# Optimization experiments

Hardware: AMD Instinct MI355X
Metric: run time of the kernel (lower is better)

## Reference

```python
import jax, jax.numpy as jnp
import numpy as np

B, S, E, H = 2, 2048, 512, 8
D = E // H  # head size = 64
LN_EPS = 1e-5


def setup_inputs() -> dict:
    key = jax.random.key(0)
    ks = jax.random.split(key, 8)
    s_in = 1.0 / np.sqrt(E)
    return {
        "x": jax.random.normal(ks[0], (B, S, E), jnp.float32),
        # per-head projection weights, stored [H, E, D] so q = x @ Wq[h]
        "Wq": jax.random.normal(ks[1], (H, E, D), jnp.float32) * s_in,
        "Wk": jax.random.normal(ks[2], (H, E, D), jnp.float32) * s_in,
        "Wv": jax.random.normal(ks[3], (H, E, D), jnp.float32) * s_in,
        "Wp": jax.random.normal(ks[4], (E, E), jnp.float32) * s_in,
        "bp": jnp.zeros((E,), jnp.float32),
        "gamma": jnp.ones((E,), jnp.float32),
        "beta": jnp.zeros((E,), jnp.float32),
        # causal mask buffer: masked_fill where mask == 0
        "mask": jnp.tril(jnp.ones((S, S), jnp.int32)),
    }


def reference(x, Wq, Wk, Wv, Wp, bp, gamma, beta, mask):
    # batched per-head projections (equivalent to the H small Linears)
    q = jnp.einsum("bse,hed->bhsd", x, Wq)
    k = jnp.einsum("bse,hed->bhsd", x, Wk)
    v = jnp.einsum("bse,hed->bhsd", x, Wv)
    # NOTE: original has NO 1/sqrt(d) scaling
    att_log = jnp.einsum("bhsd,bhtd->bhst", q, k)
    att_log = jnp.where(mask == 0, -jnp.inf, att_log)
    att = jax.nn.softmax(att_log, axis=-1)
    o = jnp.einsum("bhst,bhtd->bhsd", att, v)  # [B,H,S,D]
    # torch.cat((val, values)) prepends each head -> final order head H-1 .. 0
    o = o[:, ::-1]
    vals = o.transpose(0, 2, 1, 3).reshape(B, S, E)
    out = vals @ Wp.T + bp + x
    mu = jnp.mean(out, axis=-1, keepdims=True)
    var = jnp.var(out, axis=-1, keepdims=True)
    return (out - mu) * jax.lax.rsqrt(var + LN_EPS) * gamma + beta
```

## Files before the change

### kernel.cpp

```cpp
#include <hip/hip_runtime.h>

constexpr int Bn = 2;
constexpr int Sn = 2048;
constexpr int En = 512;
constexpr int Hn = 8;
constexpr int Dn = 64;
constexpr int Mn = Bn * Sn;

typedef short bf8 __attribute__((ext_vector_type(8)));
typedef float f32x4 __attribute__((ext_vector_type(4)));

constexpr size_t XY = (size_t)Mn * En;
constexpr size_t WT = (size_t)3 * En * En;
constexpr size_t WP = (size_t)En * En;
constexpr size_t PL = (size_t)Bn * Hn * Sn * Dn;

__device__ __forceinline__ unsigned short f2bf(float f) {
    unsigned int u = __float_as_uint(f);
    unsigned int r = 0x7FFFu + ((u >> 16) & 1u);
    return (unsigned short)((u + r) >> 16);
}
__device__ __forceinline__ float bf2f(unsigned short u) {
    return __uint_as_float(((unsigned int)u) << 16);
}
__device__ __forceinline__ void split2(float f, unsigned short& hi, unsigned short& lo) {
    hi = f2bf(f);
    lo = f2bf(f - bf2f(hi));
}

__global__ __launch_bounds__(256)
void prep(const float* __restrict__ x, const float* __restrict__ Wp,
          const float* __restrict__ Wq, const float* __restrict__ Wk,
          const float* __restrict__ Wv,
          unsigned short* __restrict__ xh, unsigned short* __restrict__ xl,
          unsigned short* __restrict__ Wph, unsigned short* __restrict__ Wpl,
          unsigned short* __restrict__ Wth, unsigned short* __restrict__ Wtl)
{
    __shared__ float t[64][65];
    const int bid = blockIdx.x;
    const int tid = threadIdx.x;

    if (bid < 1152) {
        const float* src = (bid < 1024) ? x : Wp;
        unsigned short* hp = (bid < 1024) ? xh : Wph;
        unsigned short* lp = (bid < 1024) ? xl : Wpl;
        const int blk = (bid < 1024) ? bid : (bid - 1024);
        const size_t base = ((size_t)blk * 256 + tid) * 8;
        float a[8];
        *(float4*)&a[0] = *(const float4*)(src + base);
        *(float4*)&a[4] = *(const float4*)(src + base + 4);
        unsigned short h[8], l[8];
        #pragma unroll
        for (int j = 0; j < 8; ++j) split2(a[j], h[j], l[j]);
        *(bf8*)(hp + base) = *(bf8*)&h[0];
        *(bf8*)(lp + base) = *(bf8*)&l[0];
        return;
    }

    const int idx = bid - 1152;
    const int ph = idx >> 3;
    const int proj = ph >> 3, h = ph & 7;
    const int e0 = (idx & 7) * 64;
    const float* W = (proj == 0) ? Wq : (proj == 1) ? Wk : Wv;
    const float* src = W + (size_t)h * En * Dn + (size_t)e0 * Dn;

    const int er = tid >> 2, cg = (tid & 3) * 16;
    #pragma unroll
    for (int c = 0; c < 4; ++c) {
        float4 v = *(const float4*)(src + (size_t)er * Dn + cg + 4 * c);
        t[er][cg + 4 * c + 0] = v.x;
        t[er][cg + 4 * c + 1] = v.y;
        t[er][cg + 4 * c + 2] = v.z;
        t[er][cg + 4 * c + 3] = v.w;
    }
    __syncthreads();

    const int d = tid >> 2, jg = (tid & 3) * 16;
    unsigned short h16[16], l16[16];
    #pragma unroll
    for (int j = 0; j < 16; ++j) split2(t[jg + j][d], h16[j], l16[j]);
    const size_t n = (size_t)proj * 512 + h * 64 + d;
    unsigned short* dh = Wth + n * En + e0 + jg;
    unsigned short* dl = Wtl + n * En + e0 + jg;
    *(bf8*)dh       = *(bf8*)&h16[0];
    *(bf8*)(dh + 8) = *(bf8*)&h16[8];
    *(bf8*)dl       = *(bf8*)&l16[0];
    *(bf8*)(dl + 8) = *(bf8*)&l16[8];
}

__global__ __launch_bounds__(256)
void qkv_gemm(const unsigned short* __restrict__ xh,
              const unsigned short* __restrict__ xl,
              const unsigned short* __restrict__ Wth,
              const unsigned short* __restrict__ Wtl,
              unsigned short* __restrict__ qh_g,
              unsigned short* __restrict__ ql_g,
              unsigned short* __restrict__ kh_g,
              unsigned short* __restrict__ kl_g,
              unsigned short* __restrict__ vT_g)
{
    __shared__ __align__(16) unsigned char smraw[40960];
    unsigned short (*Ah)[40] = (unsigned short(*)[40])(smraw);
    unsigned short (*Al)[40] = (unsigned short(*)[40])(smraw + 10240);
    unsigned short (*Bh)[40] = (unsigned short(*)[40])(smraw + 20480);
    unsigned short (*Bl)[40] = (unsigned short(*)[40])(smraw + 30720);
    float (*Cf)[132] = (float(*)[132])(smraw);

    const int tid = threadIdx.x;
    const int m0 = blockIdx.x * 128;
    const int n0 = blockIdx.y * 128;
    const int proj = n0 >> 9;
    const int within = n0 & 511;

    const int wave = tid >> 6, lane = tid & 63;
    const int wm = (wave >> 1) * 64, wn = (wave & 1) * 64;
    const int lm = lane & 15, quad = lane >> 4;

    const int am = tid >> 1;
    const int aks = (tid & 1) * 16;
    const unsigned short* arh = xh + (size_t)(m0 + am) * En + aks;
    const unsigned short* arl = xl + (size_t)(m0 + am) * En + aks;

    const int nn = tid & 127;
    const int bkg = (tid >> 7) * 16;
    const unsigned short* brh = Wth + (size_t)(n0 + nn) * En + bkg;
    const unsigned short* brl = Wtl + (size_t)(n0 + nn) * En + bkg;

    f32x4 acc[4][4];
    #pragma unroll
    for (int i = 0; i < 4; ++i)
        #pragma unroll
        for (int j = 0; j < 4; ++j) acc[i][j] = (f32x4){0.f, 0.f, 0.f, 0.f};

    for (int k0 = 0; k0 < En; k0 += 32) {
        *(bf8*)&Ah[am][aks]     = *(const bf8*)(arh + k0);
        *(bf8*)&Ah[am][aks + 8] = *(const bf8*)(arh + k0 + 8);
        *(bf8*)&Al[am][aks]     = *(const bf8*)(arl + k0);
        *(bf8*)&Al[am][aks + 8] = *(const bf8*)(arl + k0 + 8);
        *(bf8*)&Bh[nn][bkg]     = *(const bf8*)(brh + k0);
        *(bf8*)&Bh[nn][bkg + 8] = *(const bf8*)(brh + k0 + 8);
        *(bf8*)&Bl[nn][bkg]     = *(const bf8*)(brl + k0);
        *(bf8*)&Bl[nn][bkg + 8] = *(const bf8*)(brl + k0 + 8);
        __syncthreads();

        bf8 a_h[4], a_l[4], b_h[4], b_l[4];
        #pragma unroll
        for (int mi = 0; mi < 4; ++mi) {
            a_h[mi] = *(const bf8*)&Ah[wm + mi * 16 + lm][quad * 8];
            a_l[mi] = *(const bf8*)&Al[wm + mi * 16 + lm][quad * 8];
        }
        #pragma unroll
        for (int ni = 0; ni < 4; ++ni) {
            b_h[ni] = *(const bf8*)&Bh[wn + ni * 16 + lm][quad * 8];
            b_l[ni] = *(const bf8*)&Bl[wn + ni * 16 + lm][quad * 8];
        }
        #pragma unroll
        for (int mi = 0; mi < 4; ++mi)
            #pragma unroll
            for (int ni = 0; ni < 4; ++ni) {
                acc[mi][ni] = __builtin_amdgcn_mfma_f32_16x16x32_bf16(a_h[mi], b_h[ni], acc[mi][ni], 0, 0, 0);
                acc[mi][ni] = __builtin_amdgcn_mfma_f32_16x16x32_bf16(a_h[mi], b_l[ni], acc[mi][ni], 0, 0, 0);
                acc[mi][ni] = __builtin_amdgcn_mfma_f32_16x16x32_bf16(a_l[mi], b_h[ni], acc[mi][ni], 0, 0, 0);
            }
        __syncthreads();
    }

    if (proj < 2) {
        unsigned short* hp = (proj == 0) ? qh_g : kh_g;
        unsigned short* lp = (proj == 0) ? ql_g : kl_g;
        #pragma unroll
        for (int p = 0; p < 2; ++p) {
            #pragma unroll
            for (int dmi = 0; dmi < 2; ++dmi) {
                const int mi = 2 * p + dmi;
                #pragma unroll
                for (int ni = 0; ni < 4; ++ni)
                    #pragma unroll
                    for (int r = 0; r < 4; ++r)
                        Cf[(wave >> 1) * 32 + dmi * 16 + quad * 4 + r]
                          [wn + ni * 16 + lm] = acc[mi][ni][r];
            }
            __syncthreads();
            {
                const int lr = tid & 63;
                const int cg = (tid >> 6) * 32;
                const int m = m0 + 64 * (lr >> 5) + 32 * p + 16 * ((lr >> 4) & 1) + (lr & 15);
                const int b = m >> 11, s = m & 2047;
                const int ng = within + cg;
                const int h = ng >> 6, d = ng & 63;
                unsigned short hi[32], lo[32];
                #pragma unroll
                for (int j4 = 0; j4 < 8; ++j4) {
                    float4 v = *(const float4*)&Cf[lr][cg + 4 * j4];
                    split2(v.x, hi[4 * j4 + 0], lo[4 * j4 + 0]);
                    split2(v.y, hi[4 * j4 + 1], lo[4 * j4 + 1]);
                    split2(v.z, hi[4 * j4 + 2], lo[4 * j4 + 2]);
                    split2(v.w, hi[4 * j4 + 3], lo[4 * j4 + 3]);
                }
                const size_t base = (((size_t)(b * Hn + h) * Sn + s) * Dn) + d;
                #pragma unroll
                for (int c = 0; c < 4; ++c) {
                    *(bf8*)(hp + base + 8 * c) = *(bf8*)&hi[8 * c];
                    *(bf8*)(lp + base + 8 * c) = *(bf8*)&lo[8 * c];
                }
            }
            __syncthreads();
        }
    } else {
        #pragma unroll
        for (int mi = 0; mi < 4; ++mi) {
            const int s0 = m0 + wm + mi * 16 + quad * 4;
            const int b = s0 >> 11, s = s0 & 2047;
            #pragma unroll
            for (int ni = 0; ni < 4; ++ni) {
                const int nl = within + wn + ni * 16 + lm;
                const int h = nl >> 6, d = nl & 63;
                ushort4 pk;
                pk.x = f2bf(acc[mi][ni][0]);
                pk.y = f2bf(acc[mi][ni][1]);
                pk.z = f2bf(acc[mi][ni][2]);
                pk.w = f2bf(acc[mi][ni][3]);
                *(ushort4*)(vT_g + ((size_t)(b * Hn + h) * Dn + d) * Sn + s) = pk;
            }
        }
    }
}

__global__ __launch_bounds__(256)
void attn(const unsigned short* __restrict__ qh_g,
          const unsigned short* __restrict__ ql_g,
          const unsigned short* __restrict__ kh_g,
          const unsigned short* __restrict__ kl_g,
          const unsigned short* __restrict__ vT_g,
          unsigned short* __restrict__ Op,
          float* __restrict__ ml)
{
    extern __shared__ unsigned short sm[];
    unsigned short (*khs)[72] = (unsigned short(*)[72])(sm);
    unsigned short (*kls)[72] = (unsigned short(*)[72])(sm + 4608);
    unsigned short (*vTs)[72] = (unsigned short(*)[72])(sm + 9216);
    unsigned short (*pts)[72] = (unsigned short(*)[72])(sm + 13824);
    float* alf = (float*)(sm + 18432);

    const int bidx = blockIdx.x;
    const int r_ = bidx & 255, quarter = bidx >> 8;
    const int a_ = r_ >> 4, bh = r_ & 15;
    const int qt = (quarter & 1) ? (31 - a_) : a_;
    const int hf = quarter >> 1;
    const int n0 = (qt + 2) >> 1;
    const int its = hf ? n0 : 0;
    const int ite = hf ? (qt + 1) : n0;
    const int pslot = hf * 512 + bh * 32 + qt;

    const int tid = threadIdx.x;
    const int wave = tid >> 6, lane = tid & 63;
    const int quad = lane >> 4, lq = lane & 15;

    const unsigned short* khb = kh_g + (size_t)bh * Sn * Dn;
    const unsigned short* klb = kl_g + (size_t)bh * Sn * Dn;
    const unsigned short* vTb = vT_g + (size_t)bh * Dn * Sn;

    bf8 qfh[2], qfl[2];
    {
        const size_t qoff = ((size_t)bh * Sn + (size_t)qt * 64 + wave * 16 + lq) * Dn;
        #pragma unroll
        for (int c = 0; c < 2; ++c) {
            qfh[c] = *(const bf8*)(qh_g + qoff + c * 32 + quad * 8);
            qfl[c] = *(const bf8*)(ql_g + qoff + c * 32 + quad * 8);
        }
    }

    f32x4 accO[4];
    #pragma unroll
    for (int nj = 0; nj < 4; ++nj) accO[nj] = (f32x4){0.f, 0.f, 0.f, 0.f};
    float m = -1e30f, l = 0.f;

    const int srow = tid & 63;
    const int sdg  = tid >> 6;

    bf8 pk0, pk1, pl0, pl1, pv0, pv1;
    if (its < ite) {
        const int t0 = its * 64;
        const unsigned short* kr = khb + (size_t)(t0 + srow) * Dn + sdg * 16;
        const unsigned short* lr = klb + (size_t)(t0 + srow) * Dn + sdg * 16;
        const unsigned short* vr = vTb + (size_t)srow * Sn + t0 + sdg * 16;
        pk0 = *(const bf8*)(kr);  pk1 = *(const bf8*)(kr + 8);
        pl0 = *(const bf8*)(lr);  pl1 = *(const bf8*)(lr + 8);
        pv0 = *(const bf8*)(vr);  pv1 = *(const bf8*)(vr + 8);
    }

    for (int it = its; it < ite; ++it) {
        __syncthreads();
        *(bf8*)&khs[srow][sdg * 16]     = pk0;
        *(bf8*)&khs[srow][sdg * 16 + 8] = pk1;
        *(bf8*)&kls[srow][sdg * 16]     = pl0;
        *(bf8*)&kls[srow][sdg * 16 + 8] = pl1;
        *(bf8*)&vTs[srow][sdg * 16]     = pv0;
        *(bf8*)&vTs[srow][sdg * 16 + 8] = pv1;
        __syncthreads();

        if (it + 1 < ite) {
            const int t1 = (it + 1) * 64;
            const unsigned short* kr = khb + (size_t)(t1 + srow) * Dn + sdg * 16;
            const unsigned short* lr = klb + (size_t)(t1 + srow) * Dn + sdg * 16;
            const unsigned short* vr = vTb + (size_t)srow * Sn + t1 + sdg * 16;
            pk0 = *(const bf8*)(kr);  pk1 = *(const bf8*)(kr + 8);
            pl0 = *(const bf8*)(lr);  pl1 = *(const bf8*)(lr + 8);
            pv0 = *(const bf8*)(vr);  pv1 = *(const bf8*)(vr + 8);
        }

        f32x4 accS[4];
        #pragma unroll
        for (int mi = 0; mi < 4; ++mi) accS[mi] = (f32x4){0.f, 0.f, 0.f, 0.f};
        #pragma unroll
        for (int mi = 0; mi < 4; ++mi) {
            #pragma unroll
            for (int c = 0; c < 2; ++c) {
                bf8 ah = *(const bf8*)&khs[mi * 16 + lq][c * 32 + quad * 8];
                bf8 al = *(const bf8*)&kls[mi * 16 + lq][c * 32 + quad * 8];
                accS[mi] = __builtin_amdgcn_mfma_f32_16x16x32_bf16(ah, qfh[c], accS[mi], 0, 0, 0);
                accS[mi] = __builtin_amdgcn_mfma_f32_16x16x32_bf16(ah, qfl[c], accS[mi], 0, 0, 0);
                accS[mi] = __builtin_amdgcn_mfma_f32_16x16x32_bf16(al, qfh[c], accS[mi], 0, 0, 0);
            }
        }

        if (it == qt) {
            const int qrel = wave * 16 + lq;
            #pragma unroll
            for (int mi = 0; mi < 4; ++mi)
                #pragma unroll
                for (int r = 0; r < 4; ++r)
                    if (mi * 16 + quad * 4 + r > qrel) accS[mi][r] = -INFINITY;
        }

        float mt = -INFINITY;
        #pragma unroll
        for (int mi = 0; mi < 4; ++mi)
            #pragma unroll
            for (int r = 0; r < 4; ++r) mt = fmaxf(mt, accS[mi][r]);
        mt = fmaxf(mt, __shfl_xor(mt, 16));
        mt = fmaxf(mt, __shfl_xor(mt, 32));
        const float mnew = fmaxf(m, mt);
        const float alpha = __expf(m - mnew);
        float ls = 0.f;
        #pragma unroll
        for (int mi = 0; mi < 4; ++mi)
            #pragma unroll
            for (int r = 0; r < 4; ++r) {
                const float p = __expf(accS[mi][r] - mnew);
                accS[mi][r] = p;
                ls += p;
            }
        ls += __shfl_xor(ls, 16);
        ls += __shfl_xor(ls, 32);
        l = l * alpha + ls;
        m = mnew;

        #pragma unroll
        for (int mi = 0; mi < 4; ++mi) {
            ushort4 pk;
            pk.x = f2bf(accS[mi][0]);
            pk.y = f2bf(accS[mi][1]);
            pk.z = f2bf(accS[mi][2]);
            pk.w = f2bf(accS[mi][3]);
            *(ushort4*)&pts[wave * 16 + lq][mi * 16 + quad * 4] = pk;
        }
        if (quad == 0) alf[wave * 16 + lq] = alpha;

        {
            float4 al4 = *(const float4*)&alf[wave * 16 + quad * 4];
            #pragma unroll
            for (int nj = 0; nj < 4; ++nj) {
                accO[nj][0] *= al4.x;
                accO[nj][1] *= al4.y;
                accO[nj][2] *= al4.z;
                accO[nj][3] *= al4.w;
            }
            #pragma unroll
            for (int c = 0; c < 2; ++c) {
                bf8 pf = *(const bf8*)&pts[wave * 16 + lq][c * 32 + quad * 8];
                #pragma unroll
                for (int nj = 0; nj < 4; ++nj) {
                    bf8 vf = *(const bf8*)&vTs[nj * 16 + lq][c * 32 + quad * 8];
                    accO[nj] = __builtin_amdgcn_mfma_f32_16x16x32_bf16(pf, vf, accO[nj], 0, 0, 0);
                }
            }
        }
    }

    if (quad == 0) {
        const size_t mi_ = ((size_t)pslot * 64 + wave * 16 + lq) * 2;
        ml[mi_]     = m;
        ml[mi_ + 1] = l;
    }
    #pragma unroll
    for (int r = 0; r < 4; ++r) {
        const int q = wave * 16 + quad * 4 + r;
        unsigned short* dst = Op + ((size_t)pslot * 64 + q) * 64;
        #pragma unroll
        for (int nj = 0; nj < 4; ++nj)
            dst[nj * 16 + lq] = f2bf(accO[nj][r]);
    }
}

__global__ __launch_bounds__(256)
void out_gemm(const unsigned short* __restrict__ Op,
              const float* __restrict__ ml,
              const unsigned short* __restrict__ Wph,
              const unsigned short* __restrict__ Wpl,
              const float* __restrict__ bp,
              const float* __restrict__ x,
              float* __restrict__ outp)
{
    __shared__ unsigned short Ah[64][40], Al[64][40];
    __shared__ unsigned short Bh[128][40], Bl[128][40];

    const int tid = threadIdx.x;
    const int m0 = blockIdx.x * 64;
    const int n0 = blockIdx.y * 128;

    const int wave = tid >> 6, lane = tid & 63;
    const int wm = (wave >> 1) * 32, wn = (wave & 1) * 64;
    const int lm = lane & 15, quad = lane >> 4;

    const int am = tid >> 2;
    const int aks = (tid & 3) * 8;
    const int m_row = m0 + am;
    const int b_row = m_row >> 11, s_row = m_row & 2047;
    const int qt = s_row >> 6, qq = s_row & 63;

    float c0[8], c1[8];
    #pragma unroll
    for (int h = 0; h < 8; ++h) {
        const size_t base0 = (((size_t)(b_row * 8 + h) * 32 + qt) * 64 + qq) * 2;
        const size_t base1 = base0 + (size_t)512 * 64 * 2;
        const float m0_ = ml[base0], l0_ = ml[base0 + 1];
        const float m1_ = ml[base1], l1_ = ml[base1 + 1];
        const float mn = fmaxf(m0_, m1_);
        const float a0 = __expf(m0_ - mn), a1 = __expf(m1_ - mn);
        const float inv = 1.f / (a0 * l0_ + a1 * l1_);
        c0[h] = a0 * inv;
        c1[h] = a1 * inv;
    }

    const int bn = tid >> 1;
    const int bks = (tid & 1) * 16;
    const unsigned short* brh = Wph + (size_t)(n0 + bn) * En + bks;
    const unsigned short* brl = Wpl + (size_t)(n0 + bn) * En + bks;

    f32x4 acc[2][4];
    #pragma unroll
    for (int i = 0; i < 2; ++i)
        #pragma unroll
        for (int j = 0; j < 4; ++j) acc[i][j] = (f32x4){0.f, 0.f, 0.f, 0.f};

    for (int k0 = 0; k0 < En; k0 += 32) {
        {
            const int e0 = k0 + aks;
            const int h = 7 - (e0 >> 6);
            const int d = e0 & 63;
            const size_t p0 = (((size_t)(b_row * 8 + h) * 32 + qt) * 64 + qq) * 64 + d;
            const size_t p1 = p0 + (size_t)512 * 64 * 64;
            bf8 o0 = *(const bf8*)(Op + p0);
            bf8 o1 = *(const bf8*)(Op + p1);
            const float w0 = c0[h], w1 = c1[h];
            unsigned short hi[8], lo[8];
            #pragma unroll
            for (int j = 0; j < 8; ++j) {
                const float v = w0 * bf2f((unsigned short)o0[j]) +
                                w1 * bf2f((unsigned short)o1[j]);
                split2(v, hi[j], lo[j]);
            }
            *(bf8*)&Ah[am][aks] = *(bf8*)&hi[0];
            *(bf8*)&Al[am][aks] = *(bf8*)&lo[0];
        }
        *(bf8*)&Bh[bn][bks]     = *(const bf8*)(brh + k0);
        *(bf8*)&Bh[bn][bks + 8] = *(const bf8*)(brh + k0 + 8);
        *(bf8*)&Bl[bn][bks]     = *(const bf8*)(brl + k0);
        *(bf8*)&Bl[bn][bks + 8] = *(const bf8*)(brl + k0 + 8);
        __syncthreads();

        bf8 a_h[2], a_l[2], b_h[4], b_l[4];
        #pragma unroll
        for (int mi = 0; mi < 2; ++mi) {
            a_h[mi] = *(const bf8*)&Ah[wm + mi * 16 + lm][quad * 8];
            a_l[mi] = *(const bf8*)&Al[wm + mi * 16 + lm][quad * 8];
        }
        #pragma unroll
        for (int ni = 0; ni < 4; ++ni) {
            b_h[ni] = *(const bf8*)&Bh[wn + ni * 16 + lm][quad * 8];
            b_l[ni] = *(const bf8*)&Bl[wn + ni * 16 + lm][quad * 8];
        }
        #pragma unroll
        for (int mi = 0; mi < 2; ++mi)
            #pragma unroll
            for (int ni = 0; ni < 4; ++ni) {
                acc[mi][ni] = __builtin_amdgcn_mfma_f32_16x16x32_bf16(a_h[mi], b_h[ni], acc[mi][ni], 0, 0, 0);
                acc[mi][ni] = __builtin_amdgcn_mfma_f32_16x16x32_bf16(a_h[mi], b_l[ni], acc[mi][ni], 0, 0, 0);
                acc[mi][ni] = __builtin_amdgcn_mfma_f32_16x16x32_bf16(a_l[mi], b_h[ni], acc[mi][ni], 0, 0, 0);
            }
        __syncthreads();
    }

    #pragma unroll
    for (int mi = 0; mi < 2; ++mi) {
        #pragma unroll
        for (int r = 0; r < 4; ++r) {
            const int m = m0 + wm + mi * 16 + quad * 4 + r;
            #pragma unroll
            for (int ni = 0; ni < 4; ++ni) {
                const int n = n0 + wn + ni * 16 + lm;
                const size_t idx = (size_t)m * En + n;
                outp[idx] = acc[mi][ni][r] + bp[n] + x[idx];
            }
        }
    }
}

__global__ __launch_bounds__(256)
void ln_kernel(const float* __restrict__ outp,
               const float* __restrict__ gamma,
               const float* __restrict__ beta,
               float* __restrict__ y)
{
    const int row = blockIdx.x * 4 + (threadIdx.x >> 6);
    const int lane = threadIdx.x & 63;
    const float* r = outp + (size_t)row * En + lane * 8;

    float a[8];
    *(float4*)&a[0] = *(const float4*)(r);
    *(float4*)&a[4] = *(const float4*)(r + 4);

    float sum = 0.f, sq = 0.f;
    #pragma unroll
    for (int j = 0; j < 8; ++j) { sum += a[j]; sq += a[j] * a[j]; }
    #pragma unroll
    for (int off = 1; off < 64; off <<= 1) {
        sum += __shfl_xor(sum, off);
        sq  += __shfl_xor(sq, off);
    }
    const float mu = sum * (1.f / 512.f);
    const float var = sq * (1.f / 512.f) - mu * mu;
    const float rs = rsqrtf(var + 1e-5f);

    const float* g = gamma + lane * 8;
    const float* be = beta + lane * 8;
    float o[8];
    #pragma unroll
    for (int j = 0; j < 8; ++j)
        o[j] = (a[j] - mu) * rs * g[j] + be[j];
    float* yr = y + (size_t)row * En + lane * 8;
    *(float4*)(yr)     = *(float4*)&o[0];
    *(float4*)(yr + 4) = *(float4*)&o[4];
}

extern "C" void kernel_launch(void* const* d_in, const int* in_sizes, int n_in,
                              void* d_out, int out_size, void* d_ws, size_t ws_size,
                              hipStream_t stream)
{
    const float* x     = (const float*)d_in[0];
    const float* Wq    = (const float*)d_in[1];
    const float* Wk    = (const float*)d_in[2];
    const float* Wv    = (const float*)d_in[3];
    const float* Wp    = (const float*)d_in[4];
    const float* bp    = (const float*)d_in[5];
    const float* gamma = (const float*)d_in[6];
    const float* beta  = (const float*)d_in[7];

    float* ws   = (float*)d_ws;
    float* ml   = ws;
    float* outp = ws + XY;
    unsigned short* bfb = (unsigned short*)(ws + 2 * XY);
    unsigned short* xh  = bfb;
    unsigned short* xl  = bfb + XY;
    unsigned short* Wth = bfb + 2 * XY;
    unsigned short* Wtl = Wth + WT;
    unsigned short* Wph = Wtl + WT;
    unsigned short* Wpl = Wph + WP;
    unsigned short* qh  = Wpl + WP;
    unsigned short* ql  = qh + PL;
    unsigned short* kh  = ql + PL;
    unsigned short* kl  = kh + PL;
    unsigned short* vT  = kl + PL;
    unsigned short* Op = xh;

    const int attn_lds = 18432 * 2 + 256;
    hipFuncSetAttribute((const void*)attn,
                        hipFuncAttributeMaxDynamicSharedMemorySize, attn_lds);

    prep<<<dim3(1344), 256, 0, stream>>>(x, Wp, Wq, Wk, Wv,
                                         xh, xl, Wph, Wpl, Wth, Wtl);
    qkv_gemm<<<dim3(Mn / 128, 12), 256, 0, stream>>>(xh, xl, Wth, Wtl,
                                                     qh, ql, kh, kl, vT);
    attn<<<dim3(1024), 256, attn_lds, stream>>>(qh, ql, kh, kl, vT, Op, ml);
    out_gemm<<<dim3(Mn / 64, En / 128), 256, 0, stream>>>(Op, ml, Wph, Wpl, bp, x, outp);
    ln_kernel<<<dim3(Mn / 4), 256, 0, stream>>>(outp, gamma, beta, (float*)d_out);
}
```

Measured before the change: 182.9 us.

## Shrink QKV GEMM N-tile to one head and split-K the output projection

The QKV projection GEMM now uses 128x64 tiles, one head per block, which doubles the grid to 32x24 blocks and cuts LDS use. The intent is better occupancy and CU fill on a grid that was previously only 384 blocks. The output-projection GEMM is split along K into two halves whose partial sums go to separate buffers, and the LayerNorm kernel adds them together. This raises parallelism for the small out_gemm grid at the cost of an extra fp32 buffer write and read, and it reuses the q buffer as scratch.

```diff
diff --git a/kernel.cpp b/kernel.cpp
--- a/kernel.cpp
+++ b/kernel.cpp
@@ -99,21 +99,20 @@
               unsigned short* __restrict__ kl_g,
               unsigned short* __restrict__ vT_g)
 {
-    __shared__ __align__(16) unsigned char smraw[40960];
+    __shared__ __align__(16) unsigned char smraw[30720];
     unsigned short (*Ah)[40] = (unsigned short(*)[40])(smraw);
     unsigned short (*Al)[40] = (unsigned short(*)[40])(smraw + 10240);
     unsigned short (*Bh)[40] = (unsigned short(*)[40])(smraw + 20480);
-    unsigned short (*Bl)[40] = (unsigned short(*)[40])(smraw + 30720);
-    float (*Cf)[132] = (float(*)[132])(smraw);
+    unsigned short (*Bl)[40] = (unsigned short(*)[40])(smraw + 25600);
+    float (*Cf)[68] = (float(*)[68])(smraw);
 
     const int tid = threadIdx.x;
     const int m0 = blockIdx.x * 128;
-    const int n0 = blockIdx.y * 128;
-    const int proj = n0 >> 9;
-    const int within = n0 & 511;
+    const int ny = blockIdx.y;
+    const int proj = ny >> 3, h = ny & 7;
 
     const int wave = tid >> 6, lane = tid & 63;
-    const int wm = (wave >> 1) * 64, wn = (wave & 1) * 64;
+    const int wm = (wave >> 1) * 64, wn = (wave & 1) * 32;
     const int lm = lane & 15, quad = lane >> 4;
 
     const int am = tid >> 1;
@@ -121,43 +120,41 @@
     const unsigned short* arh = xh + (size_t)(m0 + am) * En + aks;
     const unsigned short* arl = xl + (size_t)(m0 + am) * En + aks;
 
-    const int nn = tid & 127;
-    const int bkg = (tid >> 7) * 16;
-    const unsigned short* brh = Wth + (size_t)(n0 + nn) * En + bkg;
-    const unsigned short* brl = Wtl + (size_t)(n0 + nn) * En + bkg;
-
-    f32x4 acc[4][4];
+    const int bn = tid >> 2;
+    const int bks = (tid & 3) * 8;
+    const unsigned short* brh = Wth + (size_t)(ny * 64 + bn) * En + bks;
+    const unsigned short* brl = Wtl + (size_t)(ny * 64 + bn) * En + bks;
+
+    f32x4 acc[4][2];
     #pragma unroll
     for (int i = 0; i < 4; ++i)
         #pragma unroll
-        for (int j = 0; j < 4; ++j) acc[i][j] = (f32x4){0.f, 0.f, 0.f, 0.f};
+        for (int j = 0; j < 2; ++j) acc[i][j] = (f32x4){0.f, 0.f, 0.f, 0.f};
 
     for (int k0 = 0; k0 < En; k0 += 32) {
         *(bf8*)&Ah[am][aks]     = *(const bf8*)(arh + k0);
         *(bf8*)&Ah[am][aks + 8] = *(const bf8*)(arh + k0 + 8);
         *(bf8*)&Al[am][aks]     = *(const bf8*)(arl + k0);
         *(bf8*)&Al[am][aks + 8] = *(const bf8*)(arl + k0 + 8);
-        *(bf8*)&Bh[nn][bkg]     = *(const bf8*)(brh + k0);
-        *(bf8*)&Bh[nn][bkg + 8] = *(const bf8*)(brh + k0 + 8);
-        *(bf8*)&Bl[nn][bkg]     = *(const bf8*)(brl + k0);
-        *(bf8*)&Bl[nn][bkg + 8] = *(const bf8*)(brl + k0 + 8);
+        *(bf8*)&Bh[bn][bks]     = *(const bf8*)(brh + k0);
+        *(bf8*)&Bl[bn][bks]     = *(const bf8*)(brl + k0);
         __syncthreads();
 
-        bf8 a_h[4], a_l[4], b_h[4], b_l[4];
+        bf8 a_h[4], a_l[4], b_h[2], b_l[2];
         #pragma unroll
         for (int mi = 0; mi < 4; ++mi) {
             a_h[mi] = *(const bf8*)&Ah[wm + mi * 16 + lm][quad * 8];
             a_l[mi] = *(const bf8*)&Al[wm + mi * 16 + lm][quad * 8];
         }
         #pragma unroll
-        for (int ni = 0; ni < 4; ++ni) {
+        for (int ni = 0; ni < 2; ++ni) {
             b_h[ni] = *(const bf8*)&Bh[wn + ni * 16 + lm][quad * 8];
             b_l[ni] = *(const bf8*)&Bl[wn + ni * 16 + lm][quad * 8];
         }
         #pragma unroll
         for (int mi = 0; mi < 4; ++mi)
             #pragma unroll
-            for (int ni = 0; ni < 4; ++ni) {
+            for (int ni = 0; ni < 2; ++ni) {
                 acc[mi][ni] = __builtin_amdgcn_mfma_f32_16x16x32_bf16(a_h[mi], b_h[ni], acc[mi][ni], 0, 0, 0);
                 acc[mi][ni] = __builtin_amdgcn_mfma_f32_16x16x32_bf16(a_h[mi], b_l[ni], acc[mi][ni], 0, 0, 0);
                 acc[mi][ni] = __builtin_amdgcn_mfma_f32_16x16x32_bf16(a_l[mi], b_h[ni], acc[mi][ni], 0, 0, 0);
@@ -170,39 +167,35 @@
         unsigned short* lp = (proj == 0) ? ql_g : kl_g;
         #pragma unroll
         for (int p = 0; p < 2; ++p) {
-            #pragma unroll
-            for (int dmi = 0; dmi < 2; ++dmi) {
-                const int mi = 2 * p + dmi;
+            if ((wave >> 1) == p) {
                 #pragma unroll
-                for (int ni = 0; ni < 4; ++ni)
+                for (int mi = 0; mi < 4; ++mi)
                     #pragma unroll
-                    for (int r = 0; r < 4; ++r)
-                        Cf[(wave >> 1) * 32 + dmi * 16 + quad * 4 + r]
-                          [wn + ni * 16 + lm] = acc[mi][ni][r];
+                    for (int ni = 0; ni < 2; ++ni)
+                        #pragma unroll
+                        for (int r = 0; r < 4; ++r)
+                            Cf[mi * 16 + quad * 4 + r][wn + ni * 16 + lm] = acc[mi][ni][r];
             }
             __syncthreads();
             {
                 const int lr = tid & 63;
-                const int cg = (tid >> 6) * 32;
-                const int m = m0 + 64 * (lr >> 5) + 32 * p + 16 * ((lr >> 4) & 1) + (lr & 15);
+                const int cg = (tid >> 6) * 16;
+                const int m = m0 + p * 64 + lr;
                 const int b = m >> 11, s = m & 2047;
-                const int ng = within + cg;
-                const int h = ng >> 6, d = ng & 63;
-                unsigned short hi[32], lo[32];
+                unsigned short hi[16], lo[16];
                 #pragma unroll
-                for (int j4 = 0; j4 < 8; ++j4) {
+                for (int j4 = 0; j4 < 4; ++j4) {
                     float4 v = *(const float4*)&Cf[lr][cg + 4 * j4];
                     split2(v.x, hi[4 * j4 + 0], lo[4 * j4 + 0]);
                     split2(v.y, hi[4 * j4 + 1], lo[4 * j4 + 1]);
                     split2(v.z, hi[4 * j4 + 2], lo[4 * j4 + 2]);
                     split2(v.w, hi[4 * j4 + 3], lo[4 * j4 + 3]);
                 }
-                const size_t base = (((size_t)(b * Hn + h) * Sn + s) * Dn) + d;
-                #pragma unroll
-                for (int c = 0; c < 4; ++c) {
-                    *(bf8*)(hp + base + 8 * c) = *(bf8*)&hi[8 * c];
-                    *(bf8*)(lp + base + 8 * c) = *(bf8*)&lo[8 * c];
-                }
+                const size_t base = (((size_t)(b * Hn + h) * Sn + s) * Dn) + cg;
+                *(bf8*)(hp + base)     = *(bf8*)&hi[0];
+                *(bf8*)(hp + base + 8) = *(bf8*)&hi[8];
+                *(bf8*)(lp + base)     = *(bf8*)&lo[0];
+                *(bf8*)(lp + base + 8) = *(bf8*)&lo[8];
             }
             __syncthreads();
         }
@@ -212,9 +205,8 @@
             const int s0 = m0 + wm + mi * 16 + quad * 4;
             const int b = s0 >> 11, s = s0 & 2047;
             #pragma unroll
-            for (int ni = 0; ni < 4; ++ni) {
-                const int nl = within + wn + ni * 16 + lm;
-                const int h = nl >> 6, d = nl & 63;
+            for (int ni = 0; ni < 2; ++ni) {
+                const int d = wn + ni * 16 + lm;
                 ushort4 pk;
                 pk.x = f2bf(acc[mi][ni][0]);
                 pk.y = f2bf(acc[mi][ni][1]);
@@ -410,7 +402,8 @@
               const unsigned short* __restrict__ Wpl,
               const float* __restrict__ bp,
               const float* __restrict__ x,
-              float* __restrict__ outp)
+              float* __restrict__ outp,
+              float* __restrict__ outp2)
 {
     __shared__ unsigned short Ah[64][40], Al[64][40];
     __shared__ unsigned short Bh[128][40], Bl[128][40];
@@ -418,6 +411,8 @@
     const int tid = threadIdx.x;
     const int m0 = blockIdx.x * 64;
     const int n0 = blockIdx.y * 128;
+    const int kz = blockIdx.z;
+    const int kbeg = kz * 256, kend = kbeg + 256;
 
     const int wave = tid >> 6, lane = tid & 63;
     const int wm = (wave >> 1) * 32, wn = (wave & 1) * 64;
@@ -454,7 +449,7 @@
         #pragma unroll
         for (int j = 0; j < 4; ++j) acc[i][j] = (f32x4){0.f, 0.f, 0.f, 0.f};
 
-    for (int k0 = 0; k0 < En; k0 += 32) {
+    for (int k0 = kbeg; k0 < kend; k0 += 32) {
         {
             const int e0 = k0 + aks;
             const int h = 7 - (e0 >> 6);
@@ -502,6 +497,7 @@
         __syncthreads();
     }
 
+    float* dst = kz ? outp2 : outp;
     #pragma unroll
     for (int mi = 0; mi < 2; ++mi) {
         #pragma unroll
@@ -511,7 +507,8 @@
             for (int ni = 0; ni < 4; ++ni) {
                 const int n = n0 + wn + ni * 16 + lm;
                 const size_t idx = (size_t)m * En + n;
-                outp[idx] = acc[mi][ni][r] + bp[n] + x[idx];
+                const float extra = kz ? 0.f : (bp[n] + x[idx]);
+                dst[idx] = acc[mi][ni][r] + extra;
             }
         }
     }
@@ -519,25 +516,30 @@
 
 __global__ __launch_bounds__(256)
 void ln_kernel(const float* __restrict__ outp,
+               const float* __restrict__ outp2,
                const float* __restrict__ gamma,
                const float* __restrict__ beta,
                float* __restrict__ y)
 {
     const int row = blockIdx.x * 4 + (threadIdx.x >> 6);
     const int lane = threadIdx.x & 63;
-    const float* r = outp + (size_t)row * En + lane * 8;
-
-    float a[8];
-    *(float4*)&a[0] = *(const float4*)(r);
-    *(float4*)&a[4] = *(const float4*)(r + 4);
+    const size_t off = (size_t)row * En + lane * 8;
+
+    float a[8], b2[8];
+    *(float4*)&a[0] = *(const float4*)(outp + off);
+    *(float4*)&a[4] = *(const float4*)(outp + off + 4);
+    *(float4*)&b2[0] = *(const float4*)(outp2 + off);
+    *(float4*)&b2[4] = *(const float4*)(outp2 + off + 4);
+    #pragma unroll
+    for (int j = 0; j < 8; ++j) a[j] += b2[j];
 
     float sum = 0.f, sq = 0.f;
     #pragma unroll
     for (int j = 0; j < 8; ++j) { sum += a[j]; sq += a[j] * a[j]; }
     #pragma unroll
-    for (int off = 1; off < 64; off <<= 1) {
-        sum += __shfl_xor(sum, off);
-        sq  += __shfl_xor(sq, off);
+    for (int off_ = 1; off_ < 64; off_ <<= 1) {
+        sum += __shfl_xor(sum, off_);
+        sq  += __shfl_xor(sq, off_);
     }
     const float mu = sum * (1.f / 512.f);
     const float var = sq * (1.f / 512.f) - mu * mu;
@@ -549,7 +551,7 @@
     #pragma unroll
     for (int j = 0; j < 8; ++j)
         o[j] = (a[j] - mu) * rs * g[j] + be[j];
-    float* yr = y + (size_t)row * En + lane * 8;
+    float* yr = y + off;
     *(float4*)(yr)     = *(float4*)&o[0];
     *(float4*)(yr + 4) = *(float4*)&o[4];
 }
@@ -583,6 +585,7 @@
     unsigned short* kl  = kh + PL;
     unsigned short* vT  = kl + PL;
     unsigned short* Op = xh;
+    float* outp2 = (float*)qh;
 
     const int attn_lds = 18432 * 2 + 256;
     hipFuncSetAttribute((const void*)attn,
@@ -590,9 +593,11 @@
 
     prep<<<dim3(1344), 256, 0, stream>>>(x, Wp, Wq, Wk, Wv,
                                          xh, xl, Wph, Wpl, Wth, Wtl);
-    qkv_gemm<<<dim3(Mn / 128, 12), 256, 0, stream>>>(xh, xl, Wth, Wtl,
+    qkv_gemm<<<dim3(Mn / 128, 24), 256, 0, stream>>>(xh, xl, Wth, Wtl,
                                                      qh, ql, kh, kl, vT);
     attn<<<dim3(1024), 256, attn_lds, stream>>>(qh, ql, kh, kl, vT, Op, ml);
-    out_gemm<<<dim3(Mn / 64, En / 128), 256, 0, stream>>>(Op, ml, Wph, Wpl, bp, x, outp);
-    ln_kernel<<<dim3(Mn / 4), 256, 0, stream>>>(outp, gamma, beta, (float*)d_out);
-}
+    out_gemm<<<dim3(Mn / 64, En / 128, 2), 256, 0, stream>>>(Op, ml, Wph, Wpl,
+                                                             bp, x, outp, outp2);
+    ln_kernel<<<dim3(Mn / 4), 256, 0, stream>>>(outp, outp2, gamma, beta,
+                                                (float*)d_out);
+}
```

After: 178.4 us. -2.5%, faster.
